# Performance work log

Hardware: AMD Instinct MI355X
Metric: run time of the kernel (lower is better)

## Reference

```python
import jax, jax.numpy as jnp
import numpy as np

B, C_IN, C_OUT, STYLE_DIM, H, W = 8, 512, 512, 512, 32, 32

def setup_inputs() -> dict:
    key = jax.random.key(0)
    k = jax.random.split(key, 7)
    x = jax.random.normal(k[0], (B, C_IN, H, W), dtype=jnp.float32)
    style = jax.random.normal(k[1], (B, STYLE_DIM), dtype=jnp.float32)
    noise = jax.random.normal(k[2], (B, 1, 2 * H, 2 * W), dtype=jnp.float32)
    # learned params (Conv2d weight, style_fc Linear, output bias)
    conv_w = jax.random.normal(k[3], (C_OUT, C_IN, 3, 3), dtype=jnp.float32) * 0.05
    fc_w = jax.random.normal(k[4], (C_IN, STYLE_DIM), dtype=jnp.float32) * 0.05
    fc_b = jax.random.normal(k[5], (C_IN,), dtype=jnp.float32) * 0.05
    bias = jnp.zeros((1, C_OUT, 1, 1), dtype=jnp.float32)
    return {"x": x, "style": style, "noise": noise,
            "conv_w": conv_w, "fc_w": fc_w, "fc_b": fc_b, "bias": bias}

def reference(x, style, noise, conv_w, fc_w, fc_b, bias):
    b, c, h, w = x.shape
    o = conv_w.shape[0]
    x = jnp.repeat(jnp.repeat(x, 2, axis=2), 2, axis=3)  # (B, C, 2H, 2W)
    # style modulation: (B, C)
    s = style @ fc_w.T + fc_b
    # per-sample modulated weight (B, O, C, 3, 3)
    wmod = conv_w[None] * (s[:, None, :, None, None] + 1.0)
    # demodulation
    d = jax.lax.rsqrt(jnp.sum(wmod * wmod, axis=(2, 3, 4)) + 1e-8)  # (B, O)
    wmod = wmod * d[:, :, None, None, None]
    # grouped conv: one group per batch sample
    xr = x.reshape(1, b * c, 2 * h, 2 * w)
    wr = wmod.reshape(b * o, c, 3, 3)
    y = jax.lax.conv_general_dilated(
        xr, wr, window_strides=(1, 1), padding='SAME',
        feature_group_count=b,
        dimension_numbers=('NCHW', 'OIHW', 'NCHW'))
    y = y.reshape(b, o, 2 * h, 2 * w) + bias + noise
    return jax.nn.leaky_relu(y, negative_slope=0.2)
```

## Files before the change

### kernel.cpp

```cpp
#include <hip/hip_runtime.h>

typedef short v8s __attribute__((ext_vector_type(8)));
typedef float f32x4 __attribute__((ext_vector_type(4)));
typedef unsigned short ushort_t;

#define BB    8
#define CIN   512
#define COUT  512
#define SDIM  512

#define GLDS(g, l)                                                      \
    __builtin_amdgcn_global_load_lds(                                   \
        (const __attribute__((address_space(1))) void*)(g),             \
        (__attribute__((address_space(3))) void*)(l), 16, 0, 0)

static __device__ __forceinline__ ushort_t f2bf(float f) {
    union { float f; unsigned u; } un; un.f = f;
    unsigned r = un.u + 0x7FFF + ((un.u >> 16) & 1);
    return (ushort_t)(r >> 16);
}

__global__ void k_prep1(const float* __restrict__ style, const float* __restrict__ fc_w,
                        const float* __restrict__ fc_b, float* __restrict__ m,
                        const float* __restrict__ conv_w, float* __restrict__ q,
                        ushort_t* __restrict__ Wb, float* __restrict__ guard) {
    __shared__ float sst[SDIM];
    const int bid = blockIdx.x;
    if (bid < 1024) {
        const int idx = bid * 256 + threadIdx.x;
        const int o = idx >> 9, c = idx & 511;
        float w[3][3];
        const float* wp = conv_w + idx * 9;
        float qs = 0.f;
        for (int i = 0; i < 3; i++)
            for (int j = 0; j < 3; j++) {
                float v = wp[i * 3 + j];
                w[i][j] = v;
                qs += v * v;
            }
        q[idx] = qs;
        const int ch = c >> 5, kg = (c >> 3) & 3, c8 = c & 7;
        for (int py = 0; py < 2; py++) {
            float rs[2][3];
            for (int kx = 0; kx < 3; kx++) {
                rs[0][kx] = (py == 0) ? w[0][kx] : w[0][kx] + w[1][kx];
                rs[1][kx] = (py == 0) ? w[1][kx] + w[2][kx] : w[2][kx];
            }
            for (int px = 0; px < 2; px++) {
                const int p = py * 2 + px;
                float vals[4];
                if (px == 0) {
                    vals[0] = rs[0][0];
                    vals[1] = rs[0][1] + rs[0][2];
                    vals[2] = rs[1][0];
                    vals[3] = rs[1][1] + rs[1][2];
                } else {
                    vals[0] = rs[0][0] + rs[0][1];
                    vals[1] = rs[0][2];
                    vals[2] = rs[1][0] + rs[1][1];
                    vals[3] = rs[1][2];
                }
                for (int t = 0; t < 4; t++)
                    Wb[(size_t)p * (16 * 4 * 4 * 512 * 8) + (size_t)ch * (4 * 4 * 512 * 8)
                       + ((size_t)(t * 4 + kg) * 512 + o) * 8 + c8] = f2bf(vals[t]);
            }
        }
    } else {
        const int sb = bid - 1024;
        const int bx = sb & 1, b = sb >> 1;
        if (sb == 0 && threadIdx.x < 8) guard[threadIdx.x] = 0.f;
        for (int k = threadIdx.x; k < SDIM; k += 256) sst[k] = style[b * SDIM + k];
        __syncthreads();
        const int c = bx * 256 + threadIdx.x;
        float acc = fc_b[c];
        const float* wr = fc_w + c * SDIM;
        for (int k = 0; k < SDIM; k += 4) {
            float4 w4 = *(const float4*)(wr + k);
            acc += w4.x * sst[k] + w4.y * sst[k + 1] + w4.z * sst[k + 2] + w4.w * sst[k + 3];
        }
        m[b * CIN + c] = acc + 1.0f;
    }
}

__global__ void k_prep2(const float* __restrict__ x, const float* __restrict__ m,
                        ushort_t* __restrict__ Xt, const float* __restrict__ q,
                        float* __restrict__ d) {
    __shared__ __align__(16) ushort_t lt[32 * 528];
    const int bid = blockIdx.x, t = threadIdx.x;
    if (bid < 256) {
        const int r = bid & 31, b = bid >> 5;
        for (int s = t; s < 4096; s += 256) {
            const int c = s >> 3, q4 = (s & 7) * 4;
            float4 v = *(const float4*)(x + (((size_t)(b * CIN + c) * 32 + r) * 32 + q4));
            const float mv = m[b * CIN + c];
            lt[(q4 + 0) * 528 + c] = f2bf(v.x * mv);
            lt[(q4 + 1) * 528 + c] = f2bf(v.y * mv);
            lt[(q4 + 2) * 528 + c] = f2bf(v.z * mv);
            lt[(q4 + 3) * 528 + c] = f2bf(v.w * mv);
        }
        __syncthreads();
        for (int s = t; s < 2048; s += 256) {
            const int cg = s >> 5, qq = s & 31;
            v8s v = *(v8s*)&lt[qq * 528 + cg * 8];
            *(v8s*)(Xt + (((size_t)(b * 64 + cg) * 1024) + r * 32 + qq) * 8) = v;
        }
    } else {
        const int w = (bid - 256) * 4 + (t >> 6);
        const int L = t & 63;
        const int b = w >> 9, o = w & 511;
        float4 q1 = *(const float4*)(q + o * 512 + L * 8);
        float4 q2 = *(const float4*)(q + o * 512 + L * 8 + 4);
        float4 m1 = *(const float4*)(m + b * 512 + L * 8);
        float4 m2 = *(const float4*)(m + b * 512 + L * 8 + 4);
        float acc = m1.x * m1.x * q1.x + m1.y * m1.y * q1.y + m1.z * m1.z * q1.z +
                    m1.w * m1.w * q1.w + m2.x * m2.x * q2.x + m2.y * m2.y * q2.y +
                    m2.z * m2.z * q2.z + m2.w * m2.w * q2.w;
        for (int off = 32; off; off >>= 1) acc += __shfl_down(acc, off, 64);
        if (L == 0) d[w] = rsqrtf(acc + 1e-8f);
    }
}

__global__ __launch_bounds__(512, 2) void k_gemm(
    const ushort_t* __restrict__ Xt, const ushort_t* __restrict__ Wb,
    const float* __restrict__ dmod, const float* __restrict__ bias,
    const float* __restrict__ noise, float* __restrict__ out,
    const float* __restrict__ guard) {
    __shared__ __align__(16) ushort_t Wt[4][256 * 32];
    __shared__ __align__(16) ushort_t Xs[4][256 * 32];

    const int tid = threadIdx.x;
    const int L = tid & 63;

    const int lin = blockIdx.x + 2 * blockIdx.y + 8 * blockIdx.z;
    const int log = (lin & 7) * 32 + (lin >> 3);
    const int o0 = (log & 1) * 256;
    const int n0 = ((log >> 1) & 3) * 256;
    const int zz = log >> 3;
    const int b = zz >> 2, p = zz & 3;

    const int wid = tid >> 6;
    const int py = p >> 1, px = p & 1;
    const int ry0 = py ? 0 : -1, cx0 = px ? 0 : -1;
    const int wo = (wid >> 2) * 128, wn = (wid & 3) * 64;
    const int l15 = L & 15, l4 = L >> 4;

    const ushort_t* XtB = Xt + (size_t)b * (64 * 1024 * 8);
    const ushort_t* WbP = Wb + (size_t)p * (16 * 4 * 4 * 512 * 8);

    f32x4 acc[8][4];
#pragma unroll
    for (int i = 0; i < 8; i++)
#pragma unroll
        for (int j = 0; j < 4; j++) acc[i][j] = {0.f, 0.f, 0.f, 0.f};

    auto stage1 = [&](int c0, ushort_t* wbuf, ushort_t* xbuf, int i) {
        const int slot = i * 512 + tid;
        const int row = slot >> 2;
        const int tap = (slot & 3) ^ ((row >> 1) & 3);
        const int ldo = (i * 512 + (tid & 448)) * 8;
        const ushort_t* wsrc =
            WbP + (size_t)(c0 >> 5) * (4 * 4 * 512 * 8)
            + ((size_t)((tap * 4 + ((c0 >> 3) & 3)) * 512 + o0 + row)) * 8;
        GLDS(wsrc, wbuf + ldo);
        const int pix = n0 + row;
        const int gr = (pix >> 5) + ry0 + (tap >> 1);
        const int gq = (pix & 31) + cx0 + (tap & 1);
        const ushort_t* xsrc =
            ((unsigned)gr < 32u && (unsigned)gq < 32u)
                ? XtB + ((size_t)(c0 >> 3) * 1024 + gr * 32 + gq) * 8
                : (const ushort_t*)guard;
        GLDS(xsrc, xbuf + ldo);
    };

    auto lread = [&](const ushort_t* buf, int row) -> v8s {
        const int gsel = l4 ^ ((row >> 1) & 3);
        return *(const v8s*)&buf[row * 32 + gsel * 8];
    };

#pragma unroll
    for (int pt = 0; pt < 3; ++pt) {
        stage1(pt * 8, Wt[pt], Xs[pt], 0);
        stage1(pt * 8, Wt[pt], Xs[pt], 1);
    }
    asm volatile("s_waitcnt vmcnt(8)" ::: "memory");
    __builtin_amdgcn_s_barrier();

    for (int t = 0; t < 64; ++t) {
        const ushort_t* wb = Wt[t & 3];
        const ushort_t* xb = Xs[t & 3];
        ushort_t* wnb = Wt[(t + 3) & 3];
        ushort_t* xnb = Xs[(t + 3) & 3];
        const int c0n = (t + 3) * 8;

        v8s af0[4], af1[4], bfr[4];
#pragma unroll
        for (int i = 0; i < 4; i++) af0[i] = lread(wb, wo + i * 16 + l15);
#pragma unroll
        for (int j = 0; j < 4; j++) bfr[j] = lread(xb, wn + j * 16 + l15);
#pragma unroll
        for (int i = 0; i < 4; i++) af1[i] = lread(wb, wo + 64 + i * 16 + l15);

        if (t + 3 < 64) {
            stage1(c0n, wnb, xnb, 0);
            stage1(c0n, wnb, xnb, 1);
        }

        __builtin_amdgcn_s_setprio(1);
#pragma unroll
        for (int i = 0; i < 4; i++)
#pragma unroll
            for (int j = 0; j < 4; j++)
                acc[i][j] = __builtin_amdgcn_mfma_f32_16x16x32_bf16(
                    af0[i], bfr[j], acc[i][j], 0, 0, 0);
#pragma unroll
        for (int i = 0; i < 4; i++)
#pragma unroll
            for (int j = 0; j < 4; j++)
                acc[4 + i][j] = __builtin_amdgcn_mfma_f32_16x16x32_bf16(
                    af1[i], bfr[j], acc[4 + i][j], 0, 0, 0);
        __builtin_amdgcn_s_setprio(0);

        if (t <= 61) asm volatile("s_waitcnt vmcnt(4)" ::: "memory");
        else if (t == 62) asm volatile("s_waitcnt vmcnt(0)" ::: "memory");

        __builtin_amdgcn_s_barrier();
    }

    const float* db = dmod + b * COUT;
    float nz[4];
    int ooff[4];
#pragma unroll
    for (int j = 0; j < 4; j++) {
        const int pix = n0 + wn + j * 16 + l15;
        const int Y = 2 * (pix >> 5) + py, X = 2 * (pix & 31) + px;
        nz[j] = noise[b * 4096 + Y * 64 + X];
        ooff[j] = Y * 64 + X;
    }
    float* outB = out + (size_t)b * COUT * 4096;
#pragma unroll
    for (int i = 0; i < 8; i++) {
        const int ob = o0 + wo + i * 16 + l4 * 4;
        float4 d4 = *(const float4*)(db + ob);
        float4 b4 = *(const float4*)(bias + ob);
        const float dv[4] = {d4.x, d4.y, d4.z, d4.w};
        const float bv[4] = {b4.x, b4.y, b4.z, b4.w};
#pragma unroll
        for (int reg = 0; reg < 4; reg++) {
            float* orow = outB + (size_t)(ob + reg) * 4096;
#pragma unroll
            for (int j = 0; j < 4; j++) {
                float v = acc[i][j][reg] * dv[reg] + bv[reg] + nz[j];
                orow[ooff[j]] = v > 0.f ? v : 0.2f * v;
            }
        }
    }
}

extern "C" void kernel_launch(void* const* d_in, const int* in_sizes, int n_in,
                              void* d_out, int out_size, void* d_ws, size_t ws_size,
                              hipStream_t stream) {
    const float* x      = (const float*)d_in[0];
    const float* style  = (const float*)d_in[1];
    const float* noise  = (const float*)d_in[2];
    const float* conv_w = (const float*)d_in[3];
    const float* fc_w   = (const float*)d_in[4];
    const float* fc_b   = (const float*)d_in[5];
    const float* bias   = (const float*)d_in[6];
    float* out = (float*)d_out;

    float* ws = (float*)d_ws;
    float* m     = ws;
    float* dmod  = ws + 4096;
    float* q     = ws + 8192;
    float* guard = ws + 270336;
    ushort_t* XtU = (ushort_t*)(ws + 270352);
    ushort_t* WbU = XtU + 4194304;

    k_prep1<<<1040, 256, 0, stream>>>(style, fc_w, fc_b, m, conv_w, q, WbU, guard);
    k_prep2<<<1280, 256, 0, stream>>>(x, m, XtU, q, dmod);
    k_gemm<<<dim3(2, 4, 32), 512, 0, stream>>>(XtU, WbU, dmod, bias, noise, out, guard);
}
```

Measured before the change: 182.2 us.

## Fuse prep and GEMM kernels into one cooperative persistent kernel with grid syncs

Merges the two preprocessing kernels and the implicit-GEMM conv kernel into a single cooperative kernel of 256 blocks, using grid-wide syncs between the weight/style prep, the activation transpose plus demod, and the GEMM phases. It reuses the GEMM's LDS buffers as scratch for the prep phases. The intent is to remove kernel launch gaps and the tails of the small prep kernels. The cost is two grid barriers, lower parallelism in the prep phases (256 blocks instead of about 1000), and the overhead of a cooperative launch.

```diff
diff --git a/kernel.cpp b/kernel.cpp
--- a/kernel.cpp
+++ b/kernel.cpp
@@ -1,4 +1,7 @@
 #include <hip/hip_runtime.h>
+#include <hip/hip_cooperative_groups.h>
+
+namespace cg = cooperative_groups;
 
 typedef short v8s __attribute__((ext_vector_type(8)));
 typedef float f32x4 __attribute__((ext_vector_type(4)));
@@ -20,14 +23,23 @@
     return (ushort_t)(r >> 16);
 }
 
-__global__ void k_prep1(const float* __restrict__ style, const float* __restrict__ fc_w,
-                        const float* __restrict__ fc_b, float* __restrict__ m,
-                        const float* __restrict__ conv_w, float* __restrict__ q,
-                        ushort_t* __restrict__ Wb, float* __restrict__ guard) {
-    __shared__ float sst[SDIM];
-    const int bid = blockIdx.x;
-    if (bid < 1024) {
-        const int idx = bid * 256 + threadIdx.x;
+__global__ __launch_bounds__(512, 2) void k_mega(
+    const float* __restrict__ x, const float* __restrict__ style,
+    const float* __restrict__ noise, const float* __restrict__ conv_w,
+    const float* __restrict__ fc_w, const float* __restrict__ fc_b,
+    const float* __restrict__ bias, float* __restrict__ out,
+    float* __restrict__ m, float* __restrict__ dmod, float* __restrict__ q,
+    float* __restrict__ guard, ushort_t* __restrict__ Xt,
+    ushort_t* __restrict__ Wb) {
+    __shared__ __align__(16) ushort_t Wt[4][256 * 32];
+    __shared__ __align__(16) ushort_t Xs[4][256 * 32];
+
+    const int nb = blockIdx.x;
+    const int tid = threadIdx.x;
+
+#pragma unroll
+    for (int k = 0; k < 2; ++k) {
+        const int idx = nb * 1024 + k * 512 + tid;
         const int o = idx >> 9, c = idx & 511;
         float w[3][3];
         const float* wp = conv_w + idx * 9;
@@ -65,31 +77,28 @@
                        + ((size_t)(t * 4 + kg) * 512 + o) * 8 + c8] = f2bf(vals[t]);
             }
         }
-    } else {
-        const int sb = bid - 1024;
-        const int bx = sb & 1, b = sb >> 1;
-        if (sb == 0 && threadIdx.x < 8) guard[threadIdx.x] = 0.f;
-        for (int k = threadIdx.x; k < SDIM; k += 256) sst[k] = style[b * SDIM + k];
+    }
+    if (nb < 8) {
+        float* sst = (float*)&Xs[0][0];
+        sst[tid] = style[nb * SDIM + tid];
         __syncthreads();
-        const int c = bx * 256 + threadIdx.x;
-        float acc = fc_b[c];
-        const float* wr = fc_w + c * SDIM;
-        for (int k = 0; k < SDIM; k += 4) {
-            float4 w4 = *(const float4*)(wr + k);
-            acc += w4.x * sst[k] + w4.y * sst[k + 1] + w4.z * sst[k + 2] + w4.w * sst[k + 3];
-        }
-        m[b * CIN + c] = acc + 1.0f;
-    }
-}
-
-__global__ void k_prep2(const float* __restrict__ x, const float* __restrict__ m,
-                        ushort_t* __restrict__ Xt, const float* __restrict__ q,
-                        float* __restrict__ d) {
-    __shared__ __align__(16) ushort_t lt[32 * 528];
-    const int bid = blockIdx.x, t = threadIdx.x;
-    if (bid < 256) {
-        const int r = bid & 31, b = bid >> 5;
-        for (int s = t; s < 4096; s += 256) {
+        float acc = fc_b[tid];
+        const float* wr = fc_w + tid * SDIM;
+        for (int k2 = 0; k2 < SDIM; k2 += 4) {
+            float4 w4 = *(const float4*)(wr + k2);
+            acc += w4.x * sst[k2] + w4.y * sst[k2 + 1] + w4.z * sst[k2 + 2] +
+                   w4.w * sst[k2 + 3];
+        }
+        m[nb * CIN + tid] = acc + 1.0f;
+    }
+    if (nb == 8 && tid < 8) guard[tid] = 0.f;
+    __threadfence();
+    cg::this_grid().sync();
+
+    {
+        ushort_t* lt = &Wt[0][0];
+        const int r = nb & 31, b = nb >> 5;
+        for (int s = tid; s < 4096; s += 512) {
             const int c = s >> 3, q4 = (s & 7) * 4;
             float4 v = *(const float4*)(x + (((size_t)(b * CIN + c) * 32 + r) * 32 + q4));
             const float mv = m[b * CIN + c];
@@ -99,14 +108,16 @@
             lt[(q4 + 3) * 528 + c] = f2bf(v.w * mv);
         }
         __syncthreads();
-        for (int s = t; s < 2048; s += 256) {
-            const int cg = s >> 5, qq = s & 31;
-            v8s v = *(v8s*)&lt[qq * 528 + cg * 8];
-            *(v8s*)(Xt + (((size_t)(b * 64 + cg) * 1024) + r * 32 + qq) * 8) = v;
-        }
-    } else {
-        const int w = (bid - 256) * 4 + (t >> 6);
-        const int L = t & 63;
+        for (int s = tid; s < 2048; s += 512) {
+            const int cg8 = s >> 5, qq = s & 31;
+            v8s v = *(v8s*)&lt[qq * 528 + cg8 * 8];
+            *(v8s*)(Xt + (((size_t)(b * 64 + cg8) * 1024) + r * 32 + qq) * 8) = v;
+        }
+    }
+#pragma unroll
+    for (int rr = 0; rr < 2; ++rr) {
+        const int w = nb * 16 + rr * 8 + (tid >> 6);
+        const int L = tid & 63;
         const int b = w >> 9, o = w & 511;
         float4 q1 = *(const float4*)(q + o * 512 + L * 8);
         float4 q2 = *(const float4*)(q + o * 512 + L * 8 + 4);
@@ -116,141 +127,135 @@
                     m1.w * m1.w * q1.w + m2.x * m2.x * q2.x + m2.y * m2.y * q2.y +
                     m2.z * m2.z * q2.z + m2.w * m2.w * q2.w;
         for (int off = 32; off; off >>= 1) acc += __shfl_down(acc, off, 64);
-        if (L == 0) d[w] = rsqrtf(acc + 1e-8f);
-    }
-}
-
-__global__ __launch_bounds__(512, 2) void k_gemm(
-    const ushort_t* __restrict__ Xt, const ushort_t* __restrict__ Wb,
-    const float* __restrict__ dmod, const float* __restrict__ bias,
-    const float* __restrict__ noise, float* __restrict__ out,
-    const float* __restrict__ guard) {
-    __shared__ __align__(16) ushort_t Wt[4][256 * 32];
-    __shared__ __align__(16) ushort_t Xs[4][256 * 32];
-
-    const int tid = threadIdx.x;
-    const int L = tid & 63;
-
-    const int lin = blockIdx.x + 2 * blockIdx.y + 8 * blockIdx.z;
-    const int log = (lin & 7) * 32 + (lin >> 3);
-    const int o0 = (log & 1) * 256;
-    const int n0 = ((log >> 1) & 3) * 256;
-    const int zz = log >> 3;
-    const int b = zz >> 2, p = zz & 3;
-
-    const int wid = tid >> 6;
-    const int py = p >> 1, px = p & 1;
-    const int ry0 = py ? 0 : -1, cx0 = px ? 0 : -1;
-    const int wo = (wid >> 2) * 128, wn = (wid & 3) * 64;
-    const int l15 = L & 15, l4 = L >> 4;
-
-    const ushort_t* XtB = Xt + (size_t)b * (64 * 1024 * 8);
-    const ushort_t* WbP = Wb + (size_t)p * (16 * 4 * 4 * 512 * 8);
-
-    f32x4 acc[8][4];
-#pragma unroll
-    for (int i = 0; i < 8; i++)
-#pragma unroll
-        for (int j = 0; j < 4; j++) acc[i][j] = {0.f, 0.f, 0.f, 0.f};
-
-    auto stage1 = [&](int c0, ushort_t* wbuf, ushort_t* xbuf, int i) {
-        const int slot = i * 512 + tid;
-        const int row = slot >> 2;
-        const int tap = (slot & 3) ^ ((row >> 1) & 3);
-        const int ldo = (i * 512 + (tid & 448)) * 8;
-        const ushort_t* wsrc =
-            WbP + (size_t)(c0 >> 5) * (4 * 4 * 512 * 8)
-            + ((size_t)((tap * 4 + ((c0 >> 3) & 3)) * 512 + o0 + row)) * 8;
-        GLDS(wsrc, wbuf + ldo);
-        const int pix = n0 + row;
-        const int gr = (pix >> 5) + ry0 + (tap >> 1);
-        const int gq = (pix & 31) + cx0 + (tap & 1);
-        const ushort_t* xsrc =
-            ((unsigned)gr < 32u && (unsigned)gq < 32u)
-                ? XtB + ((size_t)(c0 >> 3) * 1024 + gr * 32 + gq) * 8
-                : (const ushort_t*)guard;
-        GLDS(xsrc, xbuf + ldo);
-    };
-
-    auto lread = [&](const ushort_t* buf, int row) -> v8s {
-        const int gsel = l4 ^ ((row >> 1) & 3);
-        return *(const v8s*)&buf[row * 32 + gsel * 8];
-    };
-
-#pragma unroll
-    for (int pt = 0; pt < 3; ++pt) {
-        stage1(pt * 8, Wt[pt], Xs[pt], 0);
-        stage1(pt * 8, Wt[pt], Xs[pt], 1);
-    }
-    asm volatile("s_waitcnt vmcnt(8)" ::: "memory");
-    __builtin_amdgcn_s_barrier();
-
-    for (int t = 0; t < 64; ++t) {
-        const ushort_t* wb = Wt[t & 3];
-        const ushort_t* xb = Xs[t & 3];
-        ushort_t* wnb = Wt[(t + 3) & 3];
-        ushort_t* xnb = Xs[(t + 3) & 3];
-        const int c0n = (t + 3) * 8;
-
-        v8s af0[4], af1[4], bfr[4];
-#pragma unroll
-        for (int i = 0; i < 4; i++) af0[i] = lread(wb, wo + i * 16 + l15);
-#pragma unroll
-        for (int j = 0; j < 4; j++) bfr[j] = lread(xb, wn + j * 16 + l15);
-#pragma unroll
-        for (int i = 0; i < 4; i++) af1[i] = lread(wb, wo + 64 + i * 16 + l15);
-
-        if (t + 3 < 64) {
-            stage1(c0n, wnb, xnb, 0);
-            stage1(c0n, wnb, xnb, 1);
-        }
-
-        __builtin_amdgcn_s_setprio(1);
-#pragma unroll
-        for (int i = 0; i < 4; i++)
-#pragma unroll
-            for (int j = 0; j < 4; j++)
-                acc[i][j] = __builtin_amdgcn_mfma_f32_16x16x32_bf16(
-                    af0[i], bfr[j], acc[i][j], 0, 0, 0);
-#pragma unroll
-        for (int i = 0; i < 4; i++)
-#pragma unroll
-            for (int j = 0; j < 4; j++)
-                acc[4 + i][j] = __builtin_amdgcn_mfma_f32_16x16x32_bf16(
-                    af1[i], bfr[j], acc[4 + i][j], 0, 0, 0);
-        __builtin_amdgcn_s_setprio(0);
-
-        if (t <= 61) asm volatile("s_waitcnt vmcnt(4)" ::: "memory");
-        else if (t == 62) asm volatile("s_waitcnt vmcnt(0)" ::: "memory");
-
+        if (L == 0) dmod[w] = rsqrtf(acc + 1e-8f);
+    }
+    __threadfence();
+    cg::this_grid().sync();
+
+    {
+        const int L = tid & 63;
+
+        const int lin = nb;
+        const int log = (lin & 7) * 32 + (lin >> 3);
+        const int o0 = (log & 1) * 256;
+        const int n0 = ((log >> 1) & 3) * 256;
+        const int zz = log >> 3;
+        const int b = zz >> 2, p = zz & 3;
+
+        const int wid = tid >> 6;
+        const int py = p >> 1, px = p & 1;
+        const int ry0 = py ? 0 : -1, cx0 = px ? 0 : -1;
+        const int wo = (wid >> 2) * 128, wn = (wid & 3) * 64;
+        const int l15 = L & 15, l4 = L >> 4;
+
+        const ushort_t* XtB = Xt + (size_t)b * (64 * 1024 * 8);
+        const ushort_t* WbP = Wb + (size_t)p * (16 * 4 * 4 * 512 * 8);
+
+        f32x4 acc[8][4];
+#pragma unroll
+        for (int i = 0; i < 8; i++)
+#pragma unroll
+            for (int j = 0; j < 4; j++) acc[i][j] = {0.f, 0.f, 0.f, 0.f};
+
+        auto stage1 = [&](int c0, ushort_t* wbuf, ushort_t* xbuf, int i) {
+            const int slot = i * 512 + tid;
+            const int row = slot >> 2;
+            const int tap = (slot & 3) ^ ((row >> 1) & 3);
+            const int ldo = (i * 512 + (tid & 448)) * 8;
+            const ushort_t* wsrc =
+                WbP + (size_t)(c0 >> 5) * (4 * 4 * 512 * 8)
+                + ((size_t)((tap * 4 + ((c0 >> 3) & 3)) * 512 + o0 + row)) * 8;
+            GLDS(wsrc, wbuf + ldo);
+            const int pix = n0 + row;
+            const int gr = (pix >> 5) + ry0 + (tap >> 1);
+            const int gq = (pix & 31) + cx0 + (tap & 1);
+            const ushort_t* xsrc =
+                ((unsigned)gr < 32u && (unsigned)gq < 32u)
+                    ? XtB + ((size_t)(c0 >> 3) * 1024 + gr * 32 + gq) * 8
+                    : (const ushort_t*)guard;
+            GLDS(xsrc, xbuf + ldo);
+        };
+
+        auto lread = [&](const ushort_t* buf, int row) -> v8s {
+            const int gsel = l4 ^ ((row >> 1) & 3);
+            return *(const v8s*)&buf[row * 32 + gsel * 8];
+        };
+
+#pragma unroll
+        for (int pt = 0; pt < 3; ++pt) {
+            stage1(pt * 8, Wt[pt], Xs[pt], 0);
+            stage1(pt * 8, Wt[pt], Xs[pt], 1);
+        }
+        asm volatile("s_waitcnt vmcnt(8)" ::: "memory");
         __builtin_amdgcn_s_barrier();
-    }
-
-    const float* db = dmod + b * COUT;
-    float nz[4];
-    int ooff[4];
-#pragma unroll
-    for (int j = 0; j < 4; j++) {
-        const int pix = n0 + wn + j * 16 + l15;
-        const int Y = 2 * (pix >> 5) + py, X = 2 * (pix & 31) + px;
-        nz[j] = noise[b * 4096 + Y * 64 + X];
-        ooff[j] = Y * 64 + X;
-    }
-    float* outB = out + (size_t)b * COUT * 4096;
-#pragma unroll
-    for (int i = 0; i < 8; i++) {
-        const int ob = o0 + wo + i * 16 + l4 * 4;
-        float4 d4 = *(const float4*)(db + ob);
-        float4 b4 = *(const float4*)(bias + ob);
-        const float dv[4] = {d4.x, d4.y, d4.z, d4.w};
-        const float bv[4] = {b4.x, b4.y, b4.z, b4.w};
-#pragma unroll
-        for (int reg = 0; reg < 4; reg++) {
-            float* orow = outB + (size_t)(ob + reg) * 4096;
-#pragma unroll
-            for (int j = 0; j < 4; j++) {
-                float v = acc[i][j][reg] * dv[reg] + bv[reg] + nz[j];
-                orow[ooff[j]] = v > 0.f ? v : 0.2f * v;
+
+        for (int t = 0; t < 64; ++t) {
+            const ushort_t* wb = Wt[t & 3];
+            const ushort_t* xb = Xs[t & 3];
+            ushort_t* wnb = Wt[(t + 3) & 3];
+            ushort_t* xnb = Xs[(t + 3) & 3];
+            const int c0n = (t + 3) * 8;
+
+            v8s af0[4], af1[4], bfr[4];
+#pragma unroll
+            for (int i = 0; i < 4; i++) af0[i] = lread(wb, wo + i * 16 + l15);
+#pragma unroll
+            for (int j = 0; j < 4; j++) bfr[j] = lread(xb, wn + j * 16 + l15);
+#pragma unroll
+            for (int i = 0; i < 4; i++) af1[i] = lread(wb, wo + 64 + i * 16 + l15);
+
+            if (t + 3 < 64) {
+                stage1(c0n, wnb, xnb, 0);
+                stage1(c0n, wnb, xnb, 1);
+            }
+
+            __builtin_amdgcn_s_setprio(1);
+#pragma unroll
+            for (int i = 0; i < 4; i++)
+#pragma unroll
+                for (int j = 0; j < 4; j++)
+                    acc[i][j] = __builtin_amdgcn_mfma_f32_16x16x32_bf16(
+                        af0[i], bfr[j], acc[i][j], 0, 0, 0);
+#pragma unroll
+            for (int i = 0; i < 4; i++)
+#pragma unroll
+                for (int j = 0; j < 4; j++)
+                    acc[4 + i][j] = __builtin_amdgcn_mfma_f32_16x16x32_bf16(
+                        af1[i], bfr[j], acc[4 + i][j], 0, 0, 0);
+            __builtin_amdgcn_s_setprio(0);
+
+            if (t <= 61) asm volatile("s_waitcnt vmcnt(4)" ::: "memory");
+            else if (t == 62) asm volatile("s_waitcnt vmcnt(0)" ::: "memory");
+
+            __builtin_amdgcn_s_barrier();
+        }
+
+        const float* db = dmod + b * COUT;
+        float nz[4];
+        int ooff[4];
+#pragma unroll
+        for (int j = 0; j < 4; j++) {
+            const int pix = n0 + wn + j * 16 + l15;
+            const int Y = 2 * (pix >> 5) + py, X = 2 * (pix & 31) + px;
+            nz[j] = noise[b * 4096 + Y * 64 + X];
+            ooff[j] = Y * 64 + X;
+        }
+        float* outB = out + (size_t)b * COUT * 4096;
+#pragma unroll
+        for (int i = 0; i < 8; i++) {
+            const int ob = o0 + wo + i * 16 + l4 * 4;
+            float4 d4 = *(const float4*)(db + ob);
+            float4 b4 = *(const float4*)(bias + ob);
+            const float dv[4] = {d4.x, d4.y, d4.z, d4.w};
+            const float bv[4] = {b4.x, b4.y, b4.z, b4.w};
+#pragma unroll
+            for (int reg = 0; reg < 4; reg++) {
+                float* orow = outB + (size_t)(ob + reg) * 4096;
+#pragma unroll
+                for (int j = 0; j < 4; j++) {
+                    float v = acc[i][j][reg] * dv[reg] + bv[reg] + nz[j];
+                    orow[ooff[j]] = v > 0.f ? v : 0.2f * v;
+                }
             }
         }
     }
@@ -269,14 +274,17 @@
     float* out = (float*)d_out;
 
     float* ws = (float*)d_ws;
-    float* m     = ws;
-    float* dmod  = ws + 4096;
-    float* q     = ws + 8192;
-    float* guard = ws + 270336;
+    float* m      = ws;
+    float* dmod   = ws + 4096;
+    float* q      = ws + 8192;
+    float* guardp = ws + 270336;
     ushort_t* XtU = (ushort_t*)(ws + 270352);
     ushort_t* WbU = XtU + 4194304;
 
-    k_prep1<<<1040, 256, 0, stream>>>(style, fc_w, fc_b, m, conv_w, q, WbU, guard);
-    k_prep2<<<1280, 256, 0, stream>>>(x, m, XtU, q, dmod);
-    k_gemm<<<dim3(2, 4, 32), 512, 0, stream>>>(XtU, WbU, dmod, bias, noise, out, guard);
+    void* kargs[] = {(void*)&x,      (void*)&style, (void*)&noise, (void*)&conv_w,
+                     (void*)&fc_w,   (void*)&fc_b,  (void*)&bias,  (void*)&out,
+                     (void*)&m,      (void*)&dmod,  (void*)&q,     (void*)&guardp,
+                     (void*)&XtU,    (void*)&WbU};
+    hipLaunchCooperativeKernel((const void*)k_mega, dim3(256), dim3(512), kargs,
+                               0u, stream);
 }
```

New measurement: 384.3 us. 2.11x slower.

## Double-buffer LDS fragment reads in registers across MFMA iterations

Applied to the files above, without the earlier changes.

Unrolls the main K loop by two and loads the next step's A/B fragments from LDS into a second register set while the current step's MFMAs run, instead of reading fragments and then computing serially. The global-to-LDS prefetch is reordered to fit, and the prologue now waits for two stages to land before starting. This aims to hide LDS read latency behind matrix-core work. The cost is roughly 48 more VGPRs per thread, which could lower occupancy or cause spills, and more delicate vmcnt and barrier ordering.

```diff
diff --git a/kernel.cpp b/kernel.cpp
--- a/kernel.cpp
+++ b/kernel.cpp
@@ -171,58 +171,62 @@
                 : (const ushort_t*)guard;
         GLDS(xsrc, xbuf + ldo);
     };
+    auto stage2 = [&](int t) {
+        stage1(t * 8, Wt[t & 3], Xs[t & 3], 0);
+        stage1(t * 8, Wt[t & 3], Xs[t & 3], 1);
+    };
 
     auto lread = [&](const ushort_t* buf, int row) -> v8s {
         const int gsel = l4 ^ ((row >> 1) & 3);
         return *(const v8s*)&buf[row * 32 + gsel * 8];
     };
-
-#pragma unroll
-    for (int pt = 0; pt < 3; ++pt) {
-        stage1(pt * 8, Wt[pt], Xs[pt], 0);
-        stage1(pt * 8, Wt[pt], Xs[pt], 1);
-    }
-    asm volatile("s_waitcnt vmcnt(8)" ::: "memory");
-    __builtin_amdgcn_s_barrier();
-
-    for (int t = 0; t < 64; ++t) {
-        const ushort_t* wb = Wt[t & 3];
-        const ushort_t* xb = Xs[t & 3];
-        ushort_t* wnb = Wt[(t + 3) & 3];
-        ushort_t* xnb = Xs[(t + 3) & 3];
-        const int c0n = (t + 3) * 8;
-
-        v8s af0[4], af1[4], bfr[4];
-#pragma unroll
-        for (int i = 0; i < 4; i++) af0[i] = lread(wb, wo + i * 16 + l15);
-#pragma unroll
-        for (int j = 0; j < 4; j++) bfr[j] = lread(xb, wn + j * 16 + l15);
-#pragma unroll
-        for (int i = 0; i < 4; i++) af1[i] = lread(wb, wo + 64 + i * 16 + l15);
-
-        if (t + 3 < 64) {
-            stage1(c0n, wnb, xnb, 0);
-            stage1(c0n, wnb, xnb, 1);
-        }
-
+    auto readf = [&](int t, v8s* a0, v8s* a1, v8s* bf) {
+        const ushort_t* wb2 = Wt[t & 3];
+        const ushort_t* xb2 = Xs[t & 3];
+#pragma unroll
+        for (int i = 0; i < 4; i++) a0[i] = lread(wb2, wo + i * 16 + l15);
+#pragma unroll
+        for (int j = 0; j < 4; j++) bf[j] = lread(xb2, wn + j * 16 + l15);
+#pragma unroll
+        for (int i = 0; i < 4; i++) a1[i] = lread(wb2, wo + 64 + i * 16 + l15);
+    };
+    auto mfma_all = [&](const v8s* a0, const v8s* a1, const v8s* bf) {
         __builtin_amdgcn_s_setprio(1);
 #pragma unroll
         for (int i = 0; i < 4; i++)
 #pragma unroll
             for (int j = 0; j < 4; j++)
                 acc[i][j] = __builtin_amdgcn_mfma_f32_16x16x32_bf16(
-                    af0[i], bfr[j], acc[i][j], 0, 0, 0);
+                    a0[i], bf[j], acc[i][j], 0, 0, 0);
 #pragma unroll
         for (int i = 0; i < 4; i++)
 #pragma unroll
             for (int j = 0; j < 4; j++)
                 acc[4 + i][j] = __builtin_amdgcn_mfma_f32_16x16x32_bf16(
-                    af1[i], bfr[j], acc[4 + i][j], 0, 0, 0);
+                    a1[i], bf[j], acc[4 + i][j], 0, 0, 0);
         __builtin_amdgcn_s_setprio(0);
-
-        if (t <= 61) asm volatile("s_waitcnt vmcnt(4)" ::: "memory");
-        else if (t == 62) asm volatile("s_waitcnt vmcnt(0)" ::: "memory");
-
+    };
+
+    stage2(0);
+    stage2(1);
+    stage2(2);
+    asm volatile("s_waitcnt vmcnt(4)" ::: "memory");
+    __builtin_amdgcn_s_barrier();
+
+    v8s a0A[4], a1A[4], bA[4], a0B[4], a1B[4], bB[4];
+    readf(0, a0A, a1A, bA);
+
+    for (int t = 0; t < 64; t += 2) {
+        if (t + 3 < 64) stage2(t + 3);
+        readf(t + 1, a0B, a1B, bB);
+        mfma_all(a0A, a1A, bA);
+        if (t <= 60) asm volatile("s_waitcnt vmcnt(4)" ::: "memory");
+        __builtin_amdgcn_s_barrier();
+        if (t + 4 < 64) stage2(t + 4);
+        if (t + 2 < 64) readf(t + 2, a0A, a1A, bA);
+        mfma_all(a0B, a1B, bB);
+        if (t + 1 <= 60) asm volatile("s_waitcnt vmcnt(4)" ::: "memory");
+        else if (t + 1 == 61) asm volatile("s_waitcnt vmcnt(0)" ::: "memory");
         __builtin_amdgcn_s_barrier();
     }
 
```

New measurement: 197.4 us. +8.3%, slower.

## Halve GEMM output tile to 128x256, triple-buffer LDS, double grid

Applied to the files above, without the earlier changes.

Shrinks each k_gemm block's output tile from 256x256 to 128x256 and doubles the grid to 512 blocks. Warps are rearranged as 2x4 with a 64x64 sub-tile each, so per-thread accumulators drop from 32 to 16 vectors. The LDS ring goes from four stages (prefetch distance 3) to three (distance 2), and launch bounds now target 4 blocks per CU. The goal is more blocks and more resident waves to fill all CUs and hide latency, at the cost of lower arithmetic intensity and more redundant X tile loads.

```diff
diff --git a/kernel.cpp b/kernel.cpp
--- a/kernel.cpp
+++ b/kernel.cpp
@@ -120,56 +120,62 @@
     }
 }
 
-__global__ __launch_bounds__(512, 2) void k_gemm(
+__global__ __launch_bounds__(512, 4) void k_gemm(
     const ushort_t* __restrict__ Xt, const ushort_t* __restrict__ Wb,
     const float* __restrict__ dmod, const float* __restrict__ bias,
     const float* __restrict__ noise, float* __restrict__ out,
     const float* __restrict__ guard) {
-    __shared__ __align__(16) ushort_t Wt[4][256 * 32];
-    __shared__ __align__(16) ushort_t Xs[4][256 * 32];
+    __shared__ __align__(16) ushort_t Wt[3][128 * 32];
+    __shared__ __align__(16) ushort_t Xs[3][256 * 32];
 
     const int tid = threadIdx.x;
     const int L = tid & 63;
 
-    const int lin = blockIdx.x + 2 * blockIdx.y + 8 * blockIdx.z;
-    const int log = (lin & 7) * 32 + (lin >> 3);
-    const int o0 = (log & 1) * 256;
-    const int n0 = ((log >> 1) & 3) * 256;
-    const int zz = log >> 3;
+    const int lin = blockIdx.x + 4 * blockIdx.y + 16 * blockIdx.z;
+    const int log = (lin & 7) * 64 + (lin >> 3);
+    const int o0 = (log & 3) * 128;
+    const int n0 = ((log >> 2) & 3) * 256;
+    const int zz = log >> 4;
     const int b = zz >> 2, p = zz & 3;
 
     const int wid = tid >> 6;
     const int py = p >> 1, px = p & 1;
     const int ry0 = py ? 0 : -1, cx0 = px ? 0 : -1;
-    const int wo = (wid >> 2) * 128, wn = (wid & 3) * 64;
+    const int wo = (wid & 1) * 64, wn = (wid >> 1) * 64;
     const int l15 = L & 15, l4 = L >> 4;
 
     const ushort_t* XtB = Xt + (size_t)b * (64 * 1024 * 8);
     const ushort_t* WbP = Wb + (size_t)p * (16 * 4 * 4 * 512 * 8);
 
-    f32x4 acc[8][4];
-#pragma unroll
-    for (int i = 0; i < 8; i++)
+    f32x4 acc[4][4];
+#pragma unroll
+    for (int i = 0; i < 4; i++)
 #pragma unroll
         for (int j = 0; j < 4; j++) acc[i][j] = {0.f, 0.f, 0.f, 0.f};
 
-    auto stage1 = [&](int c0, ushort_t* wbuf, ushort_t* xbuf, int i) {
-        const int slot = i * 512 + tid;
-        const int row = slot >> 2;
-        const int tap = (slot & 3) ^ ((row >> 1) & 3);
-        const int ldo = (i * 512 + (tid & 448)) * 8;
+    auto stage_w = [&](int c0, ushort_t* wbuf) {
+        const int row = tid >> 2;
+        const int tap = (tid & 3) ^ ((row >> 1) & 3);
         const ushort_t* wsrc =
             WbP + (size_t)(c0 >> 5) * (4 * 4 * 512 * 8)
             + ((size_t)((tap * 4 + ((c0 >> 3) & 3)) * 512 + o0 + row)) * 8;
-        GLDS(wsrc, wbuf + ldo);
-        const int pix = n0 + row;
-        const int gr = (pix >> 5) + ry0 + (tap >> 1);
-        const int gq = (pix & 31) + cx0 + (tap & 1);
-        const ushort_t* xsrc =
-            ((unsigned)gr < 32u && (unsigned)gq < 32u)
-                ? XtB + ((size_t)(c0 >> 3) * 1024 + gr * 32 + gq) * 8
-                : (const ushort_t*)guard;
-        GLDS(xsrc, xbuf + ldo);
+        GLDS(wsrc, wbuf + (size_t)(tid & 448) * 8);
+    };
+    auto stage_x = [&](int c0, ushort_t* xbuf) {
+#pragma unroll
+        for (int i = 0; i < 2; i++) {
+            const int slot = i * 512 + tid;
+            const int row = slot >> 2;
+            const int tap = (slot & 3) ^ ((row >> 1) & 3);
+            const int pix = n0 + row;
+            const int gr = (pix >> 5) + ry0 + (tap >> 1);
+            const int gq = (pix & 31) + cx0 + (tap & 1);
+            const ushort_t* xsrc =
+                ((unsigned)gr < 32u && (unsigned)gq < 32u)
+                    ? XtB + ((size_t)(c0 >> 3) * 1024 + gr * 32 + gq) * 8
+                    : (const ushort_t*)guard;
+            GLDS(xsrc, xbuf + (size_t)(i * 512 + (tid & 448)) * 8);
+        }
     };
 
     auto lread = [&](const ushort_t* buf, int row) -> v8s {
@@ -177,32 +183,28 @@
         return *(const v8s*)&buf[row * 32 + gsel * 8];
     };
 
-#pragma unroll
-    for (int pt = 0; pt < 3; ++pt) {
-        stage1(pt * 8, Wt[pt], Xs[pt], 0);
-        stage1(pt * 8, Wt[pt], Xs[pt], 1);
-    }
-    asm volatile("s_waitcnt vmcnt(8)" ::: "memory");
+    stage_w(0, Wt[0]);
+    stage_x(0, Xs[0]);
+    stage_w(8, Wt[1]);
+    stage_x(8, Xs[1]);
+    asm volatile("s_waitcnt vmcnt(3)" ::: "memory");
     __builtin_amdgcn_s_barrier();
 
+    int cur = 0;
     for (int t = 0; t < 64; ++t) {
-        const ushort_t* wb = Wt[t & 3];
-        const ushort_t* xb = Xs[t & 3];
-        ushort_t* wnb = Wt[(t + 3) & 3];
-        ushort_t* xnb = Xs[(t + 3) & 3];
-        const int c0n = (t + 3) * 8;
-
-        v8s af0[4], af1[4], bfr[4];
-#pragma unroll
-        for (int i = 0; i < 4; i++) af0[i] = lread(wb, wo + i * 16 + l15);
-#pragma unroll
-        for (int j = 0; j < 4; j++) bfr[j] = lread(xb, wn + j * 16 + l15);
-#pragma unroll
-        for (int i = 0; i < 4; i++) af1[i] = lread(wb, wo + 64 + i * 16 + l15);
-
-        if (t + 3 < 64) {
-            stage1(c0n, wnb, xnb, 0);
-            stage1(c0n, wnb, xnb, 1);
+        const ushort_t* wt = Wt[cur];
+        const ushort_t* xs = Xs[cur];
+        const int stg = (cur == 0) ? 2 : cur - 1;
+
+        v8s af[4], bfr[4];
+#pragma unroll
+        for (int i = 0; i < 4; i++) af[i] = lread(wt, wo + i * 16 + l15);
+#pragma unroll
+        for (int j = 0; j < 4; j++) bfr[j] = lread(xs, wn + j * 16 + l15);
+
+        if (t + 2 < 64) {
+            stage_w((t + 2) * 8, Wt[stg]);
+            stage_x((t + 2) * 8, Xs[stg]);
         }
 
         __builtin_amdgcn_s_setprio(1);
@@ -211,19 +213,14 @@
 #pragma unroll
             for (int j = 0; j < 4; j++)
                 acc[i][j] = __builtin_amdgcn_mfma_f32_16x16x32_bf16(
-                    af0[i], bfr[j], acc[i][j], 0, 0, 0);
-#pragma unroll
-        for (int i = 0; i < 4; i++)
-#pragma unroll
-            for (int j = 0; j < 4; j++)
-                acc[4 + i][j] = __builtin_amdgcn_mfma_f32_16x16x32_bf16(
-                    af1[i], bfr[j], acc[4 + i][j], 0, 0, 0);
+                    af[i], bfr[j], acc[i][j], 0, 0, 0);
         __builtin_amdgcn_s_setprio(0);
 
-        if (t <= 61) asm volatile("s_waitcnt vmcnt(4)" ::: "memory");
+        if (t <= 61) asm volatile("s_waitcnt vmcnt(3)" ::: "memory");
         else if (t == 62) asm volatile("s_waitcnt vmcnt(0)" ::: "memory");
 
         __builtin_amdgcn_s_barrier();
+        cur = (cur == 2) ? 0 : cur + 1;
     }
 
     const float* db = dmod + b * COUT;
@@ -238,7 +235,7 @@
     }
     float* outB = out + (size_t)b * COUT * 4096;
 #pragma unroll
-    for (int i = 0; i < 8; i++) {
+    for (int i = 0; i < 4; i++) {
         const int ob = o0 + wo + i * 16 + l4 * 4;
         float4 d4 = *(const float4*)(db + ob);
         float4 b4 = *(const float4*)(bias + ob);
@@ -278,5 +275,5 @@
 
     k_prep1<<<1040, 256, 0, stream>>>(style, fc_w, fc_b, m, conv_w, q, WbU, guard);
     k_prep2<<<1280, 256, 0, stream>>>(x, m, XtU, q, dmod);
-    k_gemm<<<dim3(2, 4, 32), 512, 0, stream>>>(XtU, WbU, dmod, bias, noise, out, guard);
-}
+    k_gemm<<<dim3(4, 4, 32), 512, 0, stream>>>(XtU, WbU, dmod, bias, noise, out, guard);
+}
```

After: 189.4 us. 1.04x slower.
